# Kernel tuning notes

Hardware: AMD Instinct MI355X
Metric: run time of the kernel (lower is better)

## Reference

```python
import jax, jax.numpy as jnp
import numpy as np

R0 = 5.0
LEAK = 0.1
N_NODES = 50000
N_EDGES = 1600000
DIM_A = 32
DIM_V = 32


def setup_inputs() -> dict:
    key = jax.random.key(0)
    ks = jax.random.split(key, 10)
    s = 1.0 / np.sqrt(DIM_A)
    return {
        "r_ij": jax.random.normal(ks[0], (N_EDGES, 3), dtype=jnp.float32) * 2.0,
        "res_emb": jax.random.normal(ks[1], (N_NODES, DIM_A), dtype=jnp.float32),
        "src": jax.random.randint(ks[2], (N_EDGES,), 0, N_NODES, dtype=jnp.int64),
        "dst": jax.random.randint(ks[3], (N_EDGES,), 0, N_NODES, dtype=jnp.int64),
        "W1": jax.random.normal(ks[4], (DIM_A, DIM_A), dtype=jnp.float32) * s,
        "b1": jnp.zeros((DIM_A,), dtype=jnp.float32),
        "W2": jax.random.normal(ks[5], (DIM_A, DIM_A), dtype=jnp.float32) * s,
        "b2": jnp.zeros((DIM_A,), dtype=jnp.float32),
        "W3": jax.random.normal(ks[6], (DIM_A, DIM_A), dtype=jnp.float32) * s,
        "Wv": jax.random.normal(ks[7], (DIM_V, DIM_A), dtype=jnp.float32) * s,
    }


def _radial_encode(r, n, rmax):
    # r: [E, 3] -> [E, n]
    hn = (n + 1) // 2
    coeffs = (jnp.pi / rmax) * (1 + jnp.arange(hn) // 2).astype(r.dtype)
    dist = jnp.linalg.norm(r, axis=-1)[..., None]  # [E, 1]
    phase = coeffs * dist                           # [E, hn]
    return jnp.concatenate([jnp.cos(phase), jnp.sin(phase[..., : n - hn])], axis=-1)


def _leaky(x):
    return jnp.where(x >= 0, x, LEAK * x)


def _tens_sigmoid_vec(x):
    # Equivariant saturating nonlinearity on vectors: scale by tanh(|x|)/|x|.
    nrm = jnp.linalg.norm(x, axis=-1, keepdims=True)
    safe = jnp.where(nrm > 0, nrm, 1.0)
    return x * (jnp.tanh(nrm) / safe)


def reference(r_ij, res_emb, src, dst, W1, b1, W2, b2, W3, Wv):
    n_nodes = res_emb.shape[0]
    dim_a = W1.shape[1]
    # gather dst node features onto edges
    res_emb_j = res_emb[dst]                              # [E, dim_a]
    x = _radial_encode(r_ij, dim_a, R0) + res_emb_j       # [E, dim_a]
    h = _leaky(x @ W1.T + b1)
    h = _leaky(h @ W2.T + b2)
    rad_enc_ij = h @ W3.T                                 # [E, dim_a]
    rv = _tens_sigmoid_vec(r_ij * (7.0 / R0))             # [E, 3]
    phi_v = rad_enc_ij[..., None] * rv[:, None, :]        # [E, dim_a, 3]
    A_a = jax.ops.segment_sum(rad_enc_ij, src, num_segments=n_nodes)  # [N, dim_a]
    A_v = jax.ops.segment_sum(phi_v, src, num_segments=n_nodes)       # [N, dim_a, 3]
    out_v = jnp.einsum("nad,va->nvd", A_v, Wv)            # [N, dim_v, 3]
    return A_a, out_v
```

## Files before the change

### kernel.cpp

```cpp
#include <hip/hip_runtime.h>
#include <math.h>


#define NN 50000
#define NE 1600000
#define DA 32
#define NB (NN*4)
#define PI_R0 0.62831853071795864769f
#define SCANB_BLOCKS 782
#define RSTRIDE 34

typedef float v2f __attribute__((ext_vector_type(2)));
typedef short bf16x8 __attribute__((ext_vector_type(8)));
typedef float f32x16 __attribute__((ext_vector_type(16)));

union frag_u { unsigned u[4]; bf16x8 v; };

__device__ __forceinline__ void wsync() {
    asm volatile("s_waitcnt lgkmcnt(0)" ::: "memory");
}

__device__ __forceinline__ unsigned cvt_pk(float lo, float hi) {
    unsigned r;
    asm("v_cvt_pk_bf16_f32 %0, %1, %2" : "=v"(r) : "v"(lo), "v"(hi));
    return r;
}

__device__ __forceinline__ float leaky(float x) {
    return fmaxf(x, 0.0f) + 0.1f * fminf(x, 0.0f);
}

__device__ __forceinline__ unsigned bf_hi(float x) {
    return (__float_as_uint(x) + 0x8000u) >> 16;
}
__device__ __forceinline__ unsigned bf_pack2(float lo, float hi) {
    return bf_hi(lo) | ((__float_as_uint(hi) + 0x8000u) & 0xffff0000u);
}


__global__ __launch_bounds__(256) void k_hist(const int* __restrict__ src,
                                              int* __restrict__ counts,
                                              int* __restrict__ rank) {
    const int e = blockIdx.x * 256 + threadIdx.x;
    const int key = (src[e] << 2) | (e & 3);
    rank[e] = atomicAdd(&counts[key], 1);
}

__global__ __launch_bounds__(256) void k_scanA(const int* __restrict__ counts,
                                               int* __restrict__ bsum) {
    __shared__ int red[256];
    const int t = threadIdx.x;
    const int idx = blockIdx.x * 256 + t;
    red[t] = (idx < NB) ? counts[idx] : 0;
    __syncthreads();
    #pragma unroll
    for (int off = 128; off > 0; off >>= 1) {
        if (t < off) red[t] += red[t + off];
        __syncthreads();
    }
    if (t == 0) bsum[blockIdx.x] = red[0];
}

__global__ __launch_bounds__(1024) void k_scanB(const int* __restrict__ bsum,
                                                int* __restrict__ bbase) {
    __shared__ int s[1024];
    const int t = threadIdx.x;
    const int v = (t < SCANB_BLOCKS) ? bsum[t] : 0;
    s[t] = v;
    __syncthreads();
    #pragma unroll
    for (int off = 1; off < 1024; off <<= 1) {
        const int x = s[t] + ((t >= off) ? s[t - off] : 0);
        __syncthreads();
        s[t] = x;
        __syncthreads();
    }
    if (t < SCANB_BLOCKS) bbase[t] = s[t] - v;
}

__global__ __launch_bounds__(256) void k_scanC(const int* __restrict__ counts,
                                               const int* __restrict__ bbase,
                                               int* __restrict__ offsets) {
    __shared__ int s[256];
    const int t = threadIdx.x;
    const int idx = blockIdx.x * 256 + t;
    const int v = (idx < NB) ? counts[idx] : 0;
    s[t] = v;
    __syncthreads();
    #pragma unroll
    for (int off = 1; off < 256; off <<= 1) {
        const int x = s[t] + ((t >= off) ? s[t - off] : 0);
        __syncthreads();
        s[t] = x;
        __syncthreads();
    }
    const int excl = s[t] - v + bbase[blockIdx.x];
    if (idx < NB) offsets[idx] = excl;
    if (idx == NB - 1) offsets[NB] = excl + v;
}

__global__ __launch_bounds__(256) void k_prep(
    const float* __restrict__ r_ij,
    const int*   __restrict__ src,
    const int*   __restrict__ dst,
    const int*   __restrict__ offsets,
    const int*   __restrict__ rank,
    uint4* __restrict__ rec)
{
    const int e = blockIdx.x * 256 + threadIdx.x;
    const int s = src[e];
    const int slot = offsets[(s << 2) | (e & 3)] + rank[e];

    const float rx = r_ij[(size_t)e*3 + 0];
    const float ry = r_ij[(size_t)e*3 + 1];
    const float rz = r_ij[(size_t)e*3 + 2];
    const float dist = sqrtf(rx*rx + ry*ry + rz*rz);

    const float nq = 1.4f * dist;
    const float e2 = __expf(2.0f * nq);
    const float sc14 = (nq > 0.0f)
        ? 1.4f * (e2 - 1.0f) * __builtin_amdgcn_rcpf((e2 + 1.0f) * nq)
        : 0.0f;

    uint4 r;
    r.x = __float_as_uint(dist);
    r.y = bf_pack2(rx * sc14, ry * sc14);
    r.z = bf_hi(rz * sc14);
    r.w = (unsigned)s | ((unsigned)dst[e] << 16);
    rec[slot] = r;
}

__global__ __launch_bounds__(256) void k_embcvt(const float* __restrict__ emb,
                                                unsigned* __restrict__ emb16) {
    const int t = blockIdx.x * 256 + threadIdx.x;
    emb16[t] = bf_pack2(emb[2*t], emb[2*t + 1]);
}


__global__ __launch_bounds__(256, 2) void dt_window(
    const uint4*    __restrict__ rec,
    const unsigned* __restrict__ emb16,
    const float* __restrict__ W1, const float* __restrict__ b1,
    const float* __restrict__ W2, const float* __restrict__ b2,
    const float* __restrict__ W3,
    float* __restrict__ A_a,
    float* __restrict__ out_v)
{
    __shared__ float  xrad[4][64][RSTRIDE];
    __shared__ float4 rvn_lds[4][64];

    const int tid   = threadIdx.x;
    const int wv    = tid >> 6;
    const int lane  = tid & 63;
    const int g     = lane >> 5;
    const int m     = lane & 31;
    const int wbase = blockIdx.x * 512 + wv * 128;

    frag_u wf1[2], wf2[2], wf3[2];
    #pragma unroll
    for (int kt = 0; kt < 2; ++kt) {
        const float4 a1 = *(const float4*)&W1[m*DA + 16*kt + 4*g];
        const float4 c1 = *(const float4*)&W1[m*DA + 16*kt + 8 + 4*g];
        wf1[kt].u[0] = cvt_pk(a1.x, a1.y); wf1[kt].u[1] = cvt_pk(a1.z, a1.w);
        wf1[kt].u[2] = cvt_pk(c1.x, c1.y); wf1[kt].u[3] = cvt_pk(c1.z, c1.w);
        const float4 a2 = *(const float4*)&W2[m*DA + 16*kt + 4*g];
        const float4 c2 = *(const float4*)&W2[m*DA + 16*kt + 8 + 4*g];
        wf2[kt].u[0] = cvt_pk(a2.x, a2.y); wf2[kt].u[1] = cvt_pk(a2.z, a2.w);
        wf2[kt].u[2] = cvt_pk(c2.x, c2.y); wf2[kt].u[3] = cvt_pk(c2.z, c2.w);
        const float4 a3 = *(const float4*)&W3[m*DA + 16*kt + 4*g];
        const float4 c3 = *(const float4*)&W3[m*DA + 16*kt + 8 + 4*g];
        wf3[kt].u[0] = cvt_pk(a3.x, a3.y); wf3[kt].u[1] = cvt_pk(a3.z, a3.w);
        wf3[kt].u[2] = cvt_pk(c3.x, c3.y); wf3[kt].u[3] = cvt_pk(c3.z, c3.w);
    }

    const float4 b1q0 = *(const float4*)&b1[4*g];
    const float4 b1q1 = *(const float4*)&b1[8 + 4*g];
    const float4 b1q2 = *(const float4*)&b1[16 + 4*g];
    const float4 b1q3 = *(const float4*)&b1[24 + 4*g];
    const float4 b2q0 = *(const float4*)&b2[4*g];
    const float4 b2q1 = *(const float4*)&b2[8 + 4*g];
    const float4 b2q2 = *(const float4*)&b2[16 + 4*g];
    const float4 b2q3 = *(const float4*)&b2[24 + 4*g];

    const int p = g;
    const int i = m;
    float accA = 0.0f, a0 = 0.0f, a1 = 0.0f, a2 = 0.0f;
    int cur = -1;

    #pragma unroll
    for (int b = 0; b < 2; ++b) {
        const int slot = wbase + b*64 + lane;

        const uint4 rc = rec[slot];
        const float dist = __uint_as_float(rc.x);
        const float vx = __uint_as_float(rc.y << 16);
        const float vy = __uint_as_float(rc.y & 0xffff0000u);
        const float vz = __uint_as_float(rc.z << 16);
        const int  node = (int)(rc.w & 0xffffu);
        const int  dn   = (int)(rc.w >> 16);

        v2f xa[16];
        #pragma unroll
        for (int mm = 0; mm < 8; ++mm) {
            float sph, cph;
            __sincosf(PI_R0 * (float)(mm + 1) * dist, &sph, &cph);
            xa[mm]     = (v2f){cph, cph};
            xa[8 + mm] = (v2f){sph, sph};
        }
        const uint4* ep = (const uint4*)(emb16 + (size_t)dn * 16);
        #pragma unroll
        for (int q = 0; q < 4; ++q) {
            const uint4 u = ep[q];
            xa[q*4 + 0] += (v2f){__uint_as_float(u.x << 16), __uint_as_float(u.x & 0xffff0000u)};
            xa[q*4 + 1] += (v2f){__uint_as_float(u.y << 16), __uint_as_float(u.y & 0xffff0000u)};
            xa[q*4 + 2] += (v2f){__uint_as_float(u.z << 16), __uint_as_float(u.z & 0xffff0000u)};
            xa[q*4 + 3] += (v2f){__uint_as_float(u.w << 16), __uint_as_float(u.w & 0xffff0000u)};
        }

        rvn_lds[wv][lane] = make_float4(vx, vy, vz, __int_as_float(node));

        {
            uint2* xr = (uint2*)&xrad[wv][lane][0];
            xr[0] = make_uint2(cvt_pk(xa[0].x,  xa[0].y),  cvt_pk(xa[1].x,  xa[1].y));
            xr[1] = make_uint2(cvt_pk(xa[2].x,  xa[2].y),  cvt_pk(xa[3].x,  xa[3].y));
            xr[2] = make_uint2(cvt_pk(xa[4].x,  xa[4].y),  cvt_pk(xa[5].x,  xa[5].y));
            xr[3] = make_uint2(cvt_pk(xa[6].x,  xa[6].y),  cvt_pk(xa[7].x,  xa[7].y));
            xr[4] = make_uint2(cvt_pk(xa[8].x,  xa[8].y),  cvt_pk(xa[9].x,  xa[9].y));
            xr[5] = make_uint2(cvt_pk(xa[10].x, xa[10].y), cvt_pk(xa[11].x, xa[11].y));
            xr[6] = make_uint2(cvt_pk(xa[12].x, xa[12].y), cvt_pk(xa[13].x, xa[13].y));
            xr[7] = make_uint2(cvt_pk(xa[14].x, xa[14].y), cvt_pk(xa[15].x, xa[15].y));
        }
        wsync();

        frag_u xf[2][2];
        #pragma unroll
        for (int t = 0; t < 2; ++t) {
            const unsigned* er = (const unsigned*)&xrad[wv][32*t + m][0];
            #pragma unroll
            for (int kt = 0; kt < 2; ++kt) {
                const uint2 qa = *(const uint2*)&er[8*kt + 2*g];
                const uint2 qb = *(const uint2*)&er[8*kt + 4 + 2*g];
                xf[t][kt].u[0] = qa.x; xf[t][kt].u[1] = qa.y;
                xf[t][kt].u[2] = qb.x; xf[t][kt].u[3] = qb.y;
            }
        }

        f32x16 acc0, acc1;
        acc0[0]=b1q0.x; acc0[1]=b1q0.y; acc0[2]=b1q0.z; acc0[3]=b1q0.w;
        acc0[4]=b1q1.x; acc0[5]=b1q1.y; acc0[6]=b1q1.z; acc0[7]=b1q1.w;
        acc0[8]=b1q2.x; acc0[9]=b1q2.y; acc0[10]=b1q2.z; acc0[11]=b1q2.w;
        acc0[12]=b1q3.x; acc0[13]=b1q3.y; acc0[14]=b1q3.z; acc0[15]=b1q3.w;
        acc1 = acc0;
        acc0 = __builtin_amdgcn_mfma_f32_32x32x16_bf16(wf1[0].v, xf[0][0].v, acc0, 0, 0, 0);
        acc0 = __builtin_amdgcn_mfma_f32_32x32x16_bf16(wf1[1].v, xf[0][1].v, acc0, 0, 0, 0);
        acc1 = __builtin_amdgcn_mfma_f32_32x32x16_bf16(wf1[0].v, xf[1][0].v, acc1, 0, 0, 0);
        acc1 = __builtin_amdgcn_mfma_f32_32x32x16_bf16(wf1[1].v, xf[1][1].v, acc1, 0, 0, 0);

        frag_u hf[2][2];
        #pragma unroll
        for (int t = 0; t < 2; ++t) {
            const f32x16 a = t ? acc1 : acc0;
            float h[16];
            #pragma unroll
            for (int r = 0; r < 16; ++r) h[r] = leaky(a[r]);
            hf[t][0].u[0] = cvt_pk(h[0], h[1]);   hf[t][0].u[1] = cvt_pk(h[2], h[3]);
            hf[t][0].u[2] = cvt_pk(h[4], h[5]);   hf[t][0].u[3] = cvt_pk(h[6], h[7]);
            hf[t][1].u[0] = cvt_pk(h[8], h[9]);   hf[t][1].u[1] = cvt_pk(h[10], h[11]);
            hf[t][1].u[2] = cvt_pk(h[12], h[13]); hf[t][1].u[3] = cvt_pk(h[14], h[15]);
        }

        f32x16 c0, c1;
        c0[0]=b2q0.x; c0[1]=b2q0.y; c0[2]=b2q0.z; c0[3]=b2q0.w;
        c0[4]=b2q1.x; c0[5]=b2q1.y; c0[6]=b2q1.z; c0[7]=b2q1.w;
        c0[8]=b2q2.x; c0[9]=b2q2.y; c0[10]=b2q2.z; c0[11]=b2q2.w;
        c0[12]=b2q3.x; c0[13]=b2q3.y; c0[14]=b2q3.z; c0[15]=b2q3.w;
        c1 = c0;
        c0 = __builtin_amdgcn_mfma_f32_32x32x16_bf16(wf2[0].v, hf[0][0].v, c0, 0, 0, 0);
        c0 = __builtin_amdgcn_mfma_f32_32x32x16_bf16(wf2[1].v, hf[0][1].v, c0, 0, 0, 0);
        c1 = __builtin_amdgcn_mfma_f32_32x32x16_bf16(wf2[0].v, hf[1][0].v, c1, 0, 0, 0);
        c1 = __builtin_amdgcn_mfma_f32_32x32x16_bf16(wf2[1].v, hf[1][1].v, c1, 0, 0, 0);

        frag_u gf[2][2];
        #pragma unroll
        for (int t = 0; t < 2; ++t) {
            const f32x16 a = t ? c1 : c0;
            float h[16];
            #pragma unroll
            for (int r = 0; r < 16; ++r) h[r] = leaky(a[r]);
            gf[t][0].u[0] = cvt_pk(h[0], h[1]);   gf[t][0].u[1] = cvt_pk(h[2], h[3]);
            gf[t][0].u[2] = cvt_pk(h[4], h[5]);   gf[t][0].u[3] = cvt_pk(h[6], h[7]);
            gf[t][1].u[0] = cvt_pk(h[8], h[9]);   gf[t][1].u[1] = cvt_pk(h[10], h[11]);
            gf[t][1].u[2] = cvt_pk(h[12], h[13]); gf[t][1].u[3] = cvt_pk(h[14], h[15]);
        }

        f32x16 r0 = {}, r1 = {};
        r0 = __builtin_amdgcn_mfma_f32_32x32x16_bf16(wf3[0].v, gf[0][0].v, r0, 0, 0, 0);
        r0 = __builtin_amdgcn_mfma_f32_32x32x16_bf16(wf3[1].v, gf[0][1].v, r0, 0, 0, 0);
        r1 = __builtin_amdgcn_mfma_f32_32x32x16_bf16(wf3[0].v, gf[1][0].v, r1, 0, 0, 0);
        r1 = __builtin_amdgcn_mfma_f32_32x32x16_bf16(wf3[1].v, gf[1][1].v, r1, 0, 0, 0);

        #pragma unroll
        for (int t = 0; t < 2; ++t) {
            const f32x16 a = t ? r1 : r0;
            float* rr = &xrad[wv][32*t + m][0];
            *(float2*)&rr[4*g]          = make_float2(a[0],  a[1]);
            *(float2*)&rr[4*g + 2]      = make_float2(a[2],  a[3]);
            *(float2*)&rr[8 + 4*g]      = make_float2(a[4],  a[5]);
            *(float2*)&rr[8 + 4*g + 2]  = make_float2(a[6],  a[7]);
            *(float2*)&rr[16 + 4*g]     = make_float2(a[8],  a[9]);
            *(float2*)&rr[16 + 4*g + 2] = make_float2(a[10], a[11]);
            *(float2*)&rr[24 + 4*g]     = make_float2(a[12], a[13]);
            *(float2*)&rr[24 + 4*g + 2] = make_float2(a[14], a[15]);
        }
        wsync();

        #pragma unroll 4
        for (int l = 0; l < 64; ++l) {
            const float4 rvn = rvn_lds[wv][l];
            const int nd = __float_as_int(rvn.w);
            const float rd = xrad[wv][l][i];
            if (nd != cur) {
                if (cur >= 0) {
                    if (p == 0) {
                        atomicAdd(&A_a[cur*DA + i], accA);
                        atomicAdd(&out_v[(cur*DA + i)*3 + 0], a0);
                    } else {
                        atomicAdd(&out_v[(cur*DA + i)*3 + 1], a1);
                        atomicAdd(&out_v[(cur*DA + i)*3 + 2], a2);
                    }
                }
                accA = a0 = a1 = a2 = 0.0f;
                cur = nd;
            }
            accA += rd;
            a0 += rd * rvn.x;
            a1 += rd * rvn.y;
            a2 += rd * rvn.z;
        }
        wsync();
    }

    if (p == 0) {
        atomicAdd(&A_a[cur*DA + i], accA);
        atomicAdd(&out_v[(cur*DA + i)*3 + 0], a0);
    } else {
        atomicAdd(&out_v[(cur*DA + i)*3 + 1], a1);
        atomicAdd(&out_v[(cur*DA + i)*3 + 2], a2);
    }
}


__global__ __launch_bounds__(256) void dt_node(
    const float* __restrict__ Wv,
    float* Av_out)
{
    __shared__ float sWv[DA*DA];
    for (int i = threadIdx.x; i < DA*DA; i += 256) sWv[i] = Wv[i];
    __syncthreads();

    const int t = blockIdx.x * 256 + threadIdx.x;
    const int n = t >> 5;
    const int v = t & 31;

    const float* av = Av_out + (size_t)n * (DA*3);
    float o0 = 0.0f, o1 = 0.0f, o2 = 0.0f;
    #pragma unroll
    for (int a = 0; a < DA; ++a) {
        const float w = sWv[v*DA + a];
        o0 += w * av[a*3 + 0];
        o1 += w * av[a*3 + 1];
        o2 += w * av[a*3 + 2];
    }
    __syncthreads();
    float* o = Av_out + (size_t)n * (DA*3) + v*3;
    o[0] = o0; o[1] = o1; o[2] = o2;
}


__global__ __launch_bounds__(256) void k_hist_legacy(const int* __restrict__ src,
                                                     int* __restrict__ counts,
                                                     int* __restrict__ rank) {
    const int e = blockIdx.x * 256 + threadIdx.x;
    rank[e] = atomicAdd(&counts[src[e]], 1);
}

__global__ __launch_bounds__(256) void k_scan_legacy(const int* __restrict__ counts,
                                                     int* __restrict__ offsets) {
    __shared__ int part[256];
    const int CH = (NN + 255) / 256;
    const int t = threadIdx.x;
    const int base = t * CH;
    int s = 0;
    for (int k = 0; k < CH; ++k) { const int idx = base + k; if (idx < NN) s += counts[idx]; }
    part[t] = s;
    __syncthreads();
    if (t == 0) {
        int run = 0;
        for (int k = 0; k < 256; ++k) { const int v = part[k]; part[k] = run; run += v; }
    }
    __syncthreads();
    int run = part[t];
    for (int k = 0; k < CH; ++k) {
        const int idx = base + k;
        if (idx < NN) { offsets[idx] = run; run += counts[idx]; }
    }
    if (t == 255) offsets[NN] = run;
}

__global__ __launch_bounds__(256) void k_scatter_legacy(const int* __restrict__ src,
                                                        const int* __restrict__ offsets,
                                                        const int* __restrict__ rank,
                                                        int* __restrict__ edge_ids) {
    const int e = blockIdx.x * 256 + threadIdx.x;
    edge_ids[offsets[src[e]] + rank[e]] = e;
}

__global__ __launch_bounds__(256, 2) void dt_window_legacy(
    const float* __restrict__ r_ij,
    const float* __restrict__ res_emb,
    const int*   __restrict__ src,
    const int*   __restrict__ dst,
    const int*   __restrict__ edge_ids,
    const float* __restrict__ W1, const float* __restrict__ b1,
    const float* __restrict__ W2, const float* __restrict__ b2,
    const float* __restrict__ W3,
    float* __restrict__ A_a,
    float* __restrict__ out_v)
{
    __shared__ float  rad_lds[4][32][36];
    __shared__ float4 rvn_lds[4][64];

    const int tid  = threadIdx.x;
    const int wv   = tid >> 6;
    const int lane = tid & 63;
    const int slot = blockIdx.x * 256 + tid;

    const int eid  = edge_ids[slot];
    const int node = src[eid];

    const float rx = r_ij[(size_t)eid*3 + 0];
    const float ry = r_ij[(size_t)eid*3 + 1];
    const float rz = r_ij[(size_t)eid*3 + 2];
    const float dist = sqrtf(rx*rx + ry*ry + rz*rz);

    float xa[DA], xb[DA];
    #pragma unroll
    for (int mm = 0; mm < 8; ++mm) {
        float sph, cph;
        __sincosf(PI_R0 * (float)(mm + 1) * dist, &sph, &cph);
        xa[2*mm] = cph; xa[2*mm+1] = cph;
        xa[16+2*mm] = sph; xa[16+2*mm+1] = sph;
    }
    const float4* er = (const float4*)(res_emb + (size_t)dst[eid] * DA);
    #pragma unroll
    for (int q = 0; q < 8; ++q) {
        const float4 v = er[q];
        xa[q*4+0] += v.x; xa[q*4+1] += v.y; xa[q*4+2] += v.z; xa[q*4+3] += v.w;
    }
    #pragma unroll
    for (int i = 0; i < DA; ++i) {
        float acc = b1[i];
        #pragma unroll
        for (int j = 0; j < DA; ++j) acc += W1[i*DA + j] * xa[j];
        xb[i] = (acc >= 0.0f) ? acc : 0.1f * acc;
    }
    #pragma unroll
    for (int i = 0; i < DA; ++i) {
        float acc = b2[i];
        #pragma unroll
        for (int j = 0; j < DA; ++j) acc += W2[i*DA + j] * xb[j];
        xa[i] = (acc >= 0.0f) ? acc : 0.1f * acc;
    }
    #pragma unroll
    for (int i = 0; i < DA; ++i) {
        float acc = 0.0f;
        #pragma unroll
        for (int j = 0; j < DA; ++j) acc += W3[i*DA + j] * xa[j];
        xb[i] = acc;
    }

    const float qx = rx*1.4f, qy = ry*1.4f, qz = rz*1.4f;
    const float nq = sqrtf(qx*qx + qy*qy + qz*qz);
    const float e2 = __expf(2.0f * nq);
    const float sc = (nq > 0.0f)
        ? (e2 - 1.0f) * __builtin_amdgcn_rcpf((e2 + 1.0f) * nq)
        : 0.0f;

    rvn_lds[wv][lane] = make_float4(qx*sc, qy*sc, qz*sc, __int_as_float(node));

    const int p = lane >> 5;
    const int i = lane & 31;

    if (lane < 32) {
        float* rrow = rad_lds[wv][lane];
        #pragma unroll
        for (int q = 0; q < 8; ++q)
            *(float4*)&rrow[q*4] = make_float4(xb[q*4+0], xb[q*4+1], xb[q*4+2], xb[q*4+3]);
    }
    wsync();

    float accA = 0.0f, a0 = 0.0f, a1 = 0.0f, a2 = 0.0f;
    int cur = __float_as_int(rvn_lds[wv][0].w);

    #pragma unroll 4
    for (int l = 0; l < 32; ++l) {
        const float4 rvn = rvn_lds[wv][l];
        const int nd = __float_as_int(rvn.w);
        const float rd = rad_lds[wv][l][i];
        if (nd != cur) {
            if (p == 0) {
                atomicAdd(&A_a[cur*DA + i], accA);
                atomicAdd(&out_v[(cur*DA + i)*3 + 0], a0);
            } else {
                atomicAdd(&out_v[(cur*DA + i)*3 + 1], a1);
                atomicAdd(&out_v[(cur*DA + i)*3 + 2], a2);
            }
            accA = a0 = a1 = a2 = 0.0f;
            cur = nd;
        }
        accA += rd; a0 += rd*rvn.x; a1 += rd*rvn.y; a2 += rd*rvn.z;
    }
    wsync();
    if (lane >= 32) {
        float* rrow = rad_lds[wv][lane - 32];
        #pragma unroll
        for (int q = 0; q < 8; ++q)
            *(float4*)&rrow[q*4] = make_float4(xb[q*4+0], xb[q*4+1], xb[q*4+2], xb[q*4+3]);
    }
    wsync();
    #pragma unroll 4
    for (int l = 32; l < 64; ++l) {
        const float4 rvn = rvn_lds[wv][l];
        const int nd = __float_as_int(rvn.w);
        const float rd = rad_lds[wv][l - 32][i];
        if (nd != cur) {
            if (p == 0) {
                atomicAdd(&A_a[cur*DA + i], accA);
                atomicAdd(&out_v[(cur*DA + i)*3 + 0], a0);
            } else {
                atomicAdd(&out_v[(cur*DA + i)*3 + 1], a1);
                atomicAdd(&out_v[(cur*DA + i)*3 + 2], a2);
            }
            accA = a0 = a1 = a2 = 0.0f;
            cur = nd;
        }
        accA += rd; a0 += rd*rvn.x; a1 += rd*rvn.y; a2 += rd*rvn.z;
    }
    if (p == 0) {
        atomicAdd(&A_a[cur*DA + i], accA);
        atomicAdd(&out_v[(cur*DA + i)*3 + 0], a0);
    } else {
        atomicAdd(&out_v[(cur*DA + i)*3 + 1], a1);
        atomicAdd(&out_v[(cur*DA + i)*3 + 2], a2);
    }
}


extern "C" void kernel_launch(void* const* d_in, const int* in_sizes, int n_in,
                              void* d_out, int out_size, void* d_ws, size_t ws_size,
                              hipStream_t stream) {
    const float* r_ij    = (const float*)d_in[0];
    const float* res_emb = (const float*)d_in[1];
    const int*   src     = (const int*)d_in[2];
    const int*   dst     = (const int*)d_in[3];
    const float* W1      = (const float*)d_in[4];
    const float* b1      = (const float*)d_in[5];
    const float* W2      = (const float*)d_in[6];
    const float* b2      = (const float*)d_in[7];
    const float* W3      = (const float*)d_in[8];
    const float* Wv      = (const float*)d_in[9];

    float* A_a   = (float*)d_out;
    float* out_v = (float*)d_out + (size_t)NN * DA;

    const size_t need_new = ((size_t)NE*4 + (size_t)NN*16 + NB + NB + 1 + NE + 1024 + 1024) * sizeof(int);
    const size_t need_leg = ((size_t)NN + NN + 1 + NE + NE) * sizeof(int);

    hipMemsetAsync(d_out, 0, (size_t)out_size * sizeof(float), stream);

    if (ws_size >= need_new) {
        uint4*    rec     = (uint4*)d_ws;
        unsigned* emb16   = (unsigned*)(rec + NE);
        int*      counts  = (int*)(emb16 + (size_t)NN*16);
        int*      offsets = counts + NB;
        int*      rank    = offsets + NB + 1;
        int*      bsum    = rank + NE;
        int*      bbase   = bsum + 1024;

        hipMemsetAsync(counts, 0, (size_t)NB * sizeof(int), stream);
        k_hist  <<<NE / 256, 256, 0, stream>>>(src, counts, rank);
        k_scanA <<<SCANB_BLOCKS, 256, 0, stream>>>(counts, bsum);
        k_scanB <<<1, 1024, 0, stream>>>(bsum, bbase);
        k_scanC <<<SCANB_BLOCKS, 256, 0, stream>>>(counts, bbase, offsets);
        k_embcvt<<<(NN*16) / 256, 256, 0, stream>>>(res_emb, emb16);
        k_prep  <<<NE / 256, 256, 0, stream>>>(r_ij, src, dst, offsets, rank, rec);
        dt_window<<<NE / 512, 256, 0, stream>>>(rec, emb16,
                                                W1, b1, W2, b2, W3, A_a, out_v);
        dt_node <<<(NN * DA) / 256, 256, 0, stream>>>(Wv, out_v);
    } else if (ws_size >= need_leg) {
        int* counts   = (int*)d_ws;
        int* offsets  = counts + NN;
        int* rank     = offsets + NN + 1;
        int* edge_ids = rank + NE;

        hipMemsetAsync(counts, 0, (size_t)NN * sizeof(int), stream);
        k_hist_legacy   <<<NE / 256, 256, 0, stream>>>(src, counts, rank);
        k_scan_legacy   <<<1, 256, 0, stream>>>(counts, offsets);
        k_scatter_legacy<<<NE / 256, 256, 0, stream>>>(src, offsets, rank, edge_ids);
        dt_window_legacy<<<NE / 256, 256, 0, stream>>>(r_ij, res_emb, src, dst, edge_ids,
                                                       W1, b1, W2, b2, W3, A_a, out_v);
        dt_node         <<<(NN * DA) / 256, 256, 0, stream>>>(Wv, out_v);
    }
}
```

Baseline: 236.5 us.

## Merge setup kernels and drop sub-bucketed histogram to cut launch count

Replaces the two memsets with one zero-init kernel and folds the embedding bf16 conversion into the histogram kernel. It also drops the per-node 4-way sub-bucketing of counts, which shrinks the scan from 782 to 196 blocks, and folds the block-sum scan into scanC so k_scanB goes away. The aim is fewer launches and less scan work. In exchange, every edge of a node now hits a single atomic counter, which raises contention in the histogram and changes the order of edges within each node's segment.

New measurement: 232.0 us. About the same (-1.9%).

```diff
diff --git a/kernel.cpp b/kernel.cpp
--- a/kernel.cpp
+++ b/kernel.cpp
@@ -5,10 +5,13 @@
 #define NN 50000
 #define NE 1600000
 #define DA 32
-#define NB (NN*4)
 #define PI_R0 0.62831853071795864769f
-#define SCANB_BLOCKS 782
+#define SCAN_BLOCKS 196
+#define HIST_BLOCKS (NE/256)
+#define EMB_BLOCKS  ((NN*16)/256)
 #define RSTRIDE 34
+#define OUTQ4 1600000
+#define CNTQ4 12500
 
 typedef float v2f __attribute__((ext_vector_type(2)));
 typedef short bf16x8 __attribute__((ext_vector_type(8)));
@@ -38,20 +41,39 @@
 }
 
 
-__global__ __launch_bounds__(256) void k_hist(const int* __restrict__ src,
-                                              int* __restrict__ counts,
-                                              int* __restrict__ rank) {
-    const int e = blockIdx.x * 256 + threadIdx.x;
-    const int key = (src[e] << 2) | (e & 3);
-    rank[e] = atomicAdd(&counts[key], 1);
-}
+__global__ __launch_bounds__(256) void k_init(uint4* __restrict__ outq,
+                                              uint4* __restrict__ cntq) {
+    const uint4 z = make_uint4(0, 0, 0, 0);
+    const int stride = gridDim.x * 256;
+    for (int i = blockIdx.x * 256 + threadIdx.x; i < OUTQ4 + CNTQ4; i += stride) {
+        if (i < OUTQ4) outq[i] = z;
+        else           cntq[i - OUTQ4] = z;
+    }
+}
+
+
+__global__ __launch_bounds__(256) void k_hist_emb(const int* __restrict__ src,
+                                                  int* __restrict__ counts,
+                                                  int* __restrict__ rank,
+                                                  const float* __restrict__ emb,
+                                                  unsigned* __restrict__ emb16) {
+    const int b = blockIdx.x;
+    if (b < HIST_BLOCKS) {
+        const int e = b * 256 + threadIdx.x;
+        rank[e] = atomicAdd(&counts[src[e]], 1);
+    } else {
+        const int t = (b - HIST_BLOCKS) * 256 + threadIdx.x;
+        emb16[t] = bf_pack2(emb[2*t], emb[2*t + 1]);
+    }
+}
+
 
 __global__ __launch_bounds__(256) void k_scanA(const int* __restrict__ counts,
                                                int* __restrict__ bsum) {
     __shared__ int red[256];
     const int t = threadIdx.x;
     const int idx = blockIdx.x * 256 + t;
-    red[t] = (idx < NB) ? counts[idx] : 0;
+    red[t] = (idx < NN) ? counts[idx] : 0;
     __syncthreads();
     #pragma unroll
     for (int off = 128; off > 0; off >>= 1) {
@@ -61,30 +83,27 @@
     if (t == 0) bsum[blockIdx.x] = red[0];
 }
 
-__global__ __launch_bounds__(1024) void k_scanB(const int* __restrict__ bsum,
-                                                int* __restrict__ bbase) {
-    __shared__ int s[1024];
-    const int t = threadIdx.x;
-    const int v = (t < SCANB_BLOCKS) ? bsum[t] : 0;
-    s[t] = v;
-    __syncthreads();
-    #pragma unroll
-    for (int off = 1; off < 1024; off <<= 1) {
-        const int x = s[t] + ((t >= off) ? s[t - off] : 0);
-        __syncthreads();
-        s[t] = x;
-        __syncthreads();
-    }
-    if (t < SCANB_BLOCKS) bbase[t] = s[t] - v;
-}
-
 __global__ __launch_bounds__(256) void k_scanC(const int* __restrict__ counts,
-                                               const int* __restrict__ bbase,
+                                               const int* __restrict__ bsum,
                                                int* __restrict__ offsets) {
+    __shared__ int sb[256];
     __shared__ int s[256];
     const int t = threadIdx.x;
+
+    const int bv = (t < SCAN_BLOCKS) ? bsum[t] : 0;
+    sb[t] = bv;
+    __syncthreads();
+    #pragma unroll
+    for (int off = 1; off < 256; off <<= 1) {
+        const int x = sb[t] + ((t >= off) ? sb[t - off] : 0);
+        __syncthreads();
+        sb[t] = x;
+        __syncthreads();
+    }
+    const int base = (blockIdx.x > 0) ? sb[blockIdx.x - 1] : 0;
+
     const int idx = blockIdx.x * 256 + t;
-    const int v = (idx < NB) ? counts[idx] : 0;
+    const int v = (idx < NN) ? counts[idx] : 0;
     s[t] = v;
     __syncthreads();
     #pragma unroll
@@ -94,9 +113,9 @@
         s[t] = x;
         __syncthreads();
     }
-    const int excl = s[t] - v + bbase[blockIdx.x];
-    if (idx < NB) offsets[idx] = excl;
-    if (idx == NB - 1) offsets[NB] = excl + v;
+    const int excl = s[t] - v + base;
+    if (idx < NN) offsets[idx] = excl;
+    if (idx == NN - 1) offsets[NN] = excl + v;
 }
 
 __global__ __launch_bounds__(256) void k_prep(
@@ -109,7 +128,7 @@
 {
     const int e = blockIdx.x * 256 + threadIdx.x;
     const int s = src[e];
-    const int slot = offsets[(s << 2) | (e & 3)] + rank[e];
+    const int slot = offsets[s] + rank[e];
 
     const float rx = r_ij[(size_t)e*3 + 0];
     const float ry = r_ij[(size_t)e*3 + 1];
@@ -128,12 +147,6 @@
     r.z = bf_hi(rz * sc14);
     r.w = (unsigned)s | ((unsigned)dst[e] << 16);
     rec[slot] = r;
-}
-
-__global__ __launch_bounds__(256) void k_embcvt(const float* __restrict__ emb,
-                                                unsigned* __restrict__ emb16) {
-    const int t = blockIdx.x * 256 + threadIdx.x;
-    emb16[t] = bf_pack2(emb[2*t], emb[2*t + 1]);
 }
 
 
@@ -573,36 +586,31 @@
     float* A_a   = (float*)d_out;
     float* out_v = (float*)d_out + (size_t)NN * DA;
 
-    const size_t need_new = ((size_t)NE*4 + (size_t)NN*16 + NB + NB + 1 + NE + 1024 + 1024) * sizeof(int);
+    const size_t need_new = ((size_t)NE*4 + (size_t)NN*16 + NN + NN + 1 + NE + 256) * sizeof(int);
     const size_t need_leg = ((size_t)NN + NN + 1 + NE + NE) * sizeof(int);
-
-    hipMemsetAsync(d_out, 0, (size_t)out_size * sizeof(float), stream);
 
     if (ws_size >= need_new) {
         uint4*    rec     = (uint4*)d_ws;
         unsigned* emb16   = (unsigned*)(rec + NE);
         int*      counts  = (int*)(emb16 + (size_t)NN*16);
-        int*      offsets = counts + NB;
-        int*      rank    = offsets + NB + 1;
+        int*      offsets = counts + NN;
+        int*      rank    = offsets + NN + 1;
         int*      bsum    = rank + NE;
-        int*      bbase   = bsum + 1024;
-
-        hipMemsetAsync(counts, 0, (size_t)NB * sizeof(int), stream);
-        k_hist  <<<NE / 256, 256, 0, stream>>>(src, counts, rank);
-        k_scanA <<<SCANB_BLOCKS, 256, 0, stream>>>(counts, bsum);
-        k_scanB <<<1, 1024, 0, stream>>>(bsum, bbase);
-        k_scanC <<<SCANB_BLOCKS, 256, 0, stream>>>(counts, bbase, offsets);
-        k_embcvt<<<(NN*16) / 256, 256, 0, stream>>>(res_emb, emb16);
-        k_prep  <<<NE / 256, 256, 0, stream>>>(r_ij, src, dst, offsets, rank, rec);
-        dt_window<<<NE / 512, 256, 0, stream>>>(rec, emb16,
-                                                W1, b1, W2, b2, W3, A_a, out_v);
-        dt_node <<<(NN * DA) / 256, 256, 0, stream>>>(Wv, out_v);
+
+        k_init    <<<1024, 256, 0, stream>>>((uint4*)d_out, (uint4*)counts);
+        k_hist_emb<<<HIST_BLOCKS + EMB_BLOCKS, 256, 0, stream>>>(src, counts, rank, res_emb, emb16);
+        k_scanA   <<<SCAN_BLOCKS, 256, 0, stream>>>(counts, bsum);
+        k_scanC   <<<SCAN_BLOCKS, 256, 0, stream>>>(counts, bsum, offsets);
+        k_prep    <<<NE / 256, 256, 0, stream>>>(r_ij, src, dst, offsets, rank, rec);
+        dt_window <<<NE / 512, 256, 0, stream>>>(rec, emb16, W1, b1, W2, b2, W3, A_a, out_v);
+        dt_node   <<<(NN * DA) / 256, 256, 0, stream>>>(Wv, out_v);
     } else if (ws_size >= need_leg) {
         int* counts   = (int*)d_ws;
         int* offsets  = counts + NN;
         int* rank     = offsets + NN + 1;
         int* edge_ids = rank + NE;
 
+        hipMemsetAsync(d_out, 0, (size_t)out_size * sizeof(float), stream);
         hipMemsetAsync(counts, 0, (size_t)NN * sizeof(int), stream);
         k_hist_legacy   <<<NE / 256, 256, 0, stream>>>(src, counts, rank);
         k_scan_legacy   <<<1, 256, 0, stream>>>(counts, offsets);
```
